# Kernel optimization log

Measured on AMD Instinct MI355X. Metric: run time of the kernel, lower is better.

## Reference

```python
import jax, jax.numpy as jnp
import numpy as np
import math

D_MODEL = 512
D_STATE = 16
D_CONV = 4
EXPAND = 2
N_LAYERS = 4
VOCAB = 30522
MAXLEN = 2048
NUM_LABELS = 2
D_INNER = EXPAND * D_MODEL  # 1024
DT_RANK = math.ceil(D_MODEL / 16)  # 32
B, S = 8, 2048


def setup_inputs() -> dict:
    key = jax.random.key(0)
    ks = jax.random.split(key, 12)
    n = lambda i, shape, s=0.02: jax.random.normal(ks[i], shape, jnp.float32) * s
    dt_std = DT_RANK ** -0.5
    return {
        "input_ids": jax.random.randint(ks[0], (B, S), 0, VOCAB),
        "attention_mask": jnp.ones((B, S), jnp.int32),
        "emb": n(1, (VOCAB, D_MODEL)),
        "pos_emb": n(2, (MAXLEN, D_MODEL)),
        "in_proj_w": n(3, (N_LAYERS, 2 * D_INNER, D_MODEL)),
        "conv_w": n(4, (N_LAYERS, D_INNER, D_CONV), 0.1),
        "conv_b": jnp.zeros((N_LAYERS, D_INNER), jnp.float32),
        "x_proj_w": n(5, (N_LAYERS, DT_RANK + 2 * D_STATE, D_INNER)),
        "dt_proj_w": jax.random.uniform(ks[6], (N_LAYERS, D_INNER, DT_RANK), jnp.float32, -dt_std, dt_std),
        "dt_proj_b": jnp.zeros((N_LAYERS, D_INNER), jnp.float32),
        "A_log": jnp.log(jnp.tile(jnp.arange(1, D_STATE + 1, dtype=jnp.float32), (N_LAYERS, D_INNER, 1))),
        "Dp": jnp.ones((N_LAYERS, D_INNER), jnp.float32),
        "out_proj_w": n(7, (N_LAYERS, D_MODEL, D_INNER)),
        "ln_g": jnp.ones((N_LAYERS, D_MODEL), jnp.float32),
        "ln_b": jnp.zeros((N_LAYERS, D_MODEL), jnp.float32),
        "fn_g": jnp.ones((D_MODEL,), jnp.float32),
        "fn_b": jnp.zeros((D_MODEL,), jnp.float32),
        "cls_w1": n(8, (D_MODEL, D_MODEL)),
        "cls_b1": jnp.zeros((D_MODEL,), jnp.float32),
        "cls_w2": n(9, (NUM_LABELS, D_MODEL)),
        "cls_b2": jnp.zeros((NUM_LABELS,), jnp.float32),
    }


def _layernorm(x, g, b, eps=1e-5):
    mu = jnp.mean(x, -1, keepdims=True)
    var = jnp.mean((x - mu) ** 2, -1, keepdims=True)
    return (x - mu) * jax.lax.rsqrt(var + eps) * g + b


def _mamba_block(x, in_w, cw, cb, xw, dtw, dtb, Alog, Dv, ow):
    # x: (B, S, d_model)
    xz = jnp.einsum('bsd,ed->bse', x, in_w)  # (B,S,2*d_inner)
    xi, z = jnp.split(xz, 2, axis=-1)
    # causal depthwise conv1d (left pad d_conv-1, valid conv)
    xp = jnp.pad(xi, ((0, 0), (D_CONV - 1, 0), (0, 0)))
    rhs = jnp.transpose(cw)[:, None, :]  # (d_conv, 1, d_inner)
    xc = jax.lax.conv_general_dilated(
        xp, rhs, (1,), 'VALID',
        dimension_numbers=('NWC', 'WIO', 'NWC'),
        feature_group_count=D_INNER) + cb
    xc = jax.nn.silu(xc)  # (B,S,d_inner)
    x_dbl = jnp.einsum('bsd,ed->bse', xc, xw)
    dt = x_dbl[..., :DT_RANK]
    Bm = x_dbl[..., DT_RANK:DT_RANK + D_STATE]
    Cm = x_dbl[..., DT_RANK + D_STATE:]
    dt = jax.nn.softplus(jnp.einsum('bsr,dr->bsd', dt, dtw) + dtb)  # (B,S,d_inner)
    A = -jnp.exp(Alog)  # (d_inner, d_state)

    def step(h, inp):
        x_t, dt_t, B_t, C_t = inp  # (B,d_inner),(B,d_inner),(B,d_state),(B,d_state)
        dA = jnp.exp(dt_t[:, :, None] * A[None])
        h = dA * h + (dt_t[:, :, None] * B_t[:, None, :]) * x_t[:, :, None]
        y_t = jnp.einsum('bds,bs->bd', h, C_t) + Dv * x_t
        return h, y_t

    h0 = jnp.zeros((x.shape[0], D_INNER, D_STATE), x.dtype)
    xs = (jnp.swapaxes(xc, 0, 1), jnp.swapaxes(dt, 0, 1),
          jnp.swapaxes(Bm, 0, 1), jnp.swapaxes(Cm, 0, 1))
    _, ys = jax.lax.scan(step, h0, xs)
    y = jnp.swapaxes(ys, 0, 1)  # (B,S,d_inner)
    y = y * jax.nn.silu(z)
    return jnp.einsum('bse,de->bsd', y, ow)


def reference(input_ids, attention_mask, emb, pos_emb, in_proj_w, conv_w, conv_b,
              x_proj_w, dt_proj_w, dt_proj_b, A_log, Dp, out_proj_w,
              ln_g, ln_b, fn_g, fn_b, cls_w1, cls_b1, cls_w2, cls_b2):
    seq_len = input_ids.shape[1]
    x = emb[input_ids] + pos_emb[:seq_len][None]
    for l in range(N_LAYERS):
        res = x
        x = _mamba_block(x, in_proj_w[l], conv_w[l], conv_b[l], x_proj_w[l],
                         dt_proj_w[l], dt_proj_b[l], A_log[l], Dp[l], out_proj_w[l])
        x = _layernorm(x + res, ln_g[l], ln_b[l])
    x = _layernorm(x, fn_g, fn_b)
    mask = attention_mask[:, :, None].astype(x.dtype)
    pooled = (x * mask).sum(1) / jnp.clip(mask.sum(1), 1e-9)
    h = jax.nn.gelu(pooled @ cls_w1.T + cls_b1, approximate=False)
    logits = h @ cls_w2.T + cls_b2
    return logits
```

## Files before the change

kernel.cpp:

```cpp
#include <hip/hip_runtime.h>
#include <math.h>

#define BATCH   8
#define S_LEN   2048
#define TOK     (BATCH*S_LEN)
#define DM      512
#define DI      1024
#define DST     16
#define DTR     32
#define NL      4
#define NLAB    2
#define NC      32
#define LC      (S_LEN/NC)

typedef _Float16 f16;
typedef _Float16 f16x8 __attribute__((ext_vector_type(8)));
typedef _Float16 f16x4 __attribute__((ext_vector_type(4)));
typedef float    f32x4 __attribute__((ext_vector_type(4)));

static constexpr size_t X_OFF     = 0;
static constexpr size_t XH_OFF    = 8388608;
static constexpr size_t XZH_OFF   = 12582912;
static constexpr size_t XCH_OFF   = 29360128;
static constexpr size_t XDBL_OFF  = 37748736;
static constexpr size_t DTH_OFF   = 38797312;
static constexpr size_t YH_OFF    = 47185920;
static constexpr size_t SDT_OFF   = 55574528;
static constexpr size_t WH_OFF    = 57802752;
static constexpr size_t XDH_OFF   = 61210624;
static constexpr size_t POOL_OFF  = 61734912;
static constexpr size_t H1_OFF    = POOL_OFF + 4096;

static constexpr size_t INWH_H  = 0;
static constexpr size_t XWH_H   = 4194304;
static constexpr size_t OWH_H   = 4456448;
static constexpr size_t DTWH_H  = 6553600;

__device__ __forceinline__ float softplus_fast(float x) {
    return fmaxf(x, 0.f) + __logf(1.f + __expf(-fabsf(x)));
}
__device__ __forceinline__ float silu_f(float x) {
    return x / (1.f + __expf(-x));
}

__device__ __forceinline__ void pow_tree(float w, float p[16]) {
    p[0] = w;           p[1] = w * w;       p[2] = p[1] * w;    p[3] = p[1] * p[1];
    p[4] = p[3] * w;    p[5] = p[3] * p[1]; p[6] = p[3] * p[2]; p[7] = p[3] * p[3];
    p[8] = p[7] * w;    p[9] = p[7] * p[1]; p[10] = p[7] * p[2]; p[11] = p[7] * p[3];
    p[12] = p[7] * p[4]; p[13] = p[7] * p[5]; p[14] = p[7] * p[6]; p[15] = p[7] * p[7];
}

__device__ __forceinline__ void gl_lds16(const void* g, void* l) {
    __builtin_amdgcn_global_load_lds(
        (const __attribute__((address_space(1))) void*)g,
        (__attribute__((address_space(3))) void*)l, 16, 0, 0);
}

__global__ __launch_bounds__(256)
void f2h_kernel(const float* __restrict__ src, f16* __restrict__ dst, int n8)
{
    int i = blockIdx.x * 256 + threadIdx.x;
    if (i >= n8) return;
    float4 a = ((const float4*)src)[i*2];
    float4 b = ((const float4*)src)[i*2+1];
    f16x8 o;
    o[0]=(f16)a.x; o[1]=(f16)a.y; o[2]=(f16)a.z; o[3]=(f16)a.w;
    o[4]=(f16)b.x; o[5]=(f16)b.y; o[6]=(f16)b.z; o[7]=(f16)b.w;
    *(f16x8*)(dst + (size_t)i*8) = o;
}

__global__ __launch_bounds__(256)
void dtw_pad_kernel(const float* __restrict__ src, f16* __restrict__ dst)
{
    int i = blockIdx.x * 256 + threadIdx.x;
    int c = i & 63;
    int row = i >> 6;
    dst[i] = (c < DTR) ? (f16)src[(size_t)row * DTR + c] : (f16)0.f;
}

__global__ __launch_bounds__(256)
void embed_kernel(const int* __restrict__ ids, const float* __restrict__ emb,
                  const float* __restrict__ pos, float* __restrict__ x,
                  f16* __restrict__ xh)
{
    int i = blockIdx.x * 256 + threadIdx.x;
    int t = i >> 7;
    int q = i & 127;
    int s = t & (S_LEN - 1);
    int id = ids[t];
    const float4 e = *(const float4*)(emb + ((size_t)id * DM) + q * 4);
    const float4 p = *(const float4*)(pos + ((size_t)s * DM) + q * 4);
    float4 o; o.x = e.x + p.x; o.y = e.y + p.y; o.z = e.z + p.z; o.w = e.w + p.w;
    *(float4*)(x + (size_t)t * DM + q * 4) = o;
    f16x4 h; h[0]=(f16)o.x; h[1]=(f16)o.y; h[2]=(f16)o.z; h[3]=(f16)o.w;
    *(f16x4*)(xh + (size_t)t * DM + q * 4) = h;
}

template<int BM,int BN,int EPI,typename OutT>
__global__ __launch_bounds__(256)
void gemm_h(const f16* __restrict__ A, const f16* __restrict__ B, OutT* __restrict__ C,
            const float* __restrict__ bias, f16* __restrict__ hcopy,
            int M, int N, int K, int lda, int ldb, int ldc)
{
    constexpr int BK = 64;
    constexpr int MI = BM / 32;
    constexpr int NI = BN / 32;
    __shared__ __align__(16) f16 As[2][BM * BK];
    __shared__ __align__(16) f16 Bs[2][BN * BK];

    const int tid  = threadIdx.x;
    const int wid  = tid >> 6, lane = tid & 63;
    const int wr   = wid >> 1, wc = wid & 1;
    const int m0   = blockIdx.x * BM, n0 = blockIdx.y * BN;
    const int srow = lane >> 3;
    const int scol = ((lane & 7) ^ (srow & 7)) * 8;
    constexpr int CPA = (BM / 8) / 4;
    constexpr int CPB = (BN / 8) / 4;

    f32x4 acc[MI][NI] = {};

    auto stage = [&](int buf, int kt) {
        #pragma unroll
        for (int i = 0; i < CPA; i++) {
            int ch = wid * CPA + i;
            gl_lds16(A + (size_t)(m0 + ch*8 + srow) * lda + kt + scol, &As[buf][ch*512]);
        }
        #pragma unroll
        for (int i = 0; i < CPB; i++) {
            int ch = wid * CPB + i;
            gl_lds16(B + (size_t)(n0 + ch*8 + srow) * ldb + kt + scol, &Bs[buf][ch*512]);
        }
    };
    auto compute = [&](int buf) {
        #pragma unroll
        for (int ks = 0; ks < 2; ks++) {
            f16x8 a[MI], b[NI];
            #pragma unroll
            for (int mi = 0; mi < MI; mi++) {
                int r = wr*MI*16 + mi*16 + (lane&15);
                int s = (ks*4 + (lane>>4)) ^ (r & 7);
                a[mi] = *(const f16x8*)(&As[buf][r*64 + s*8]);
            }
            #pragma unroll
            for (int ni = 0; ni < NI; ni++) {
                int r = wc*NI*16 + ni*16 + (lane&15);
                int s = (ks*4 + (lane>>4)) ^ (r & 7);
                b[ni] = *(const f16x8*)(&Bs[buf][r*64 + s*8]);
            }
            #pragma unroll
            for (int mi = 0; mi < MI; mi++)
                #pragma unroll
                for (int ni = 0; ni < NI; ni++)
                    acc[mi][ni] = __builtin_amdgcn_mfma_f32_16x16x32_f16(a[mi], b[ni], acc[mi][ni], 0, 0, 0);
        }
    };

    stage(0, 0);
    __syncthreads();
    int cur = 0;
    for (int kt = BK; kt < K; kt += BK) {
        stage(cur ^ 1, kt);
        compute(cur);
        __syncthreads();
        cur ^= 1;
    }
    compute(cur);

    const int cl = lane & 15, rh = lane >> 4;
    #pragma unroll
    for (int mi = 0; mi < MI; mi++) {
        #pragma unroll
        for (int ni = 0; ni < NI; ni++) {
            int col = n0 + wc*NI*16 + ni*16 + cl;
            #pragma unroll
            for (int r = 0; r < 4; r++) {
                int row = m0 + wr*MI*16 + mi*16 + rh*4 + r;
                float v = acc[mi][ni][r];
                if (EPI == 1) {
                    v = softplus_fast(v + bias[col]);
                    C[(size_t)row * ldc + col] = (OutT)v;
                } else {
                    C[(size_t)row * ldc + col] = (OutT)v;
                    if (EPI == 2) hcopy[(size_t)row * ldc + col] = (f16)v;
                }
            }
        }
    }
}

template<typename OutT>
__global__ __launch_bounds__(512)
void gemm_h8(const f16* __restrict__ A, const f16* __restrict__ B, OutT* __restrict__ C,
             int M, int N, int K, int lda, int ldb, int ldc, int nbn)
{
    constexpr int BK = 64;
    __shared__ __align__(16) f16 As[2][256 * BK];
    __shared__ __align__(16) f16 Bs[2][256 * BK];

    const int tid  = threadIdx.x;
    const int wid  = tid >> 6, lane = tid & 63;
    const int wr   = wid >> 2, wc = wid & 3;
    const int nwg = gridDim.x;
    const int xcd = blockIdx.x & 7, j = blockIdx.x >> 3;
    const int per_xcd_m = (nwg >> 3) / nbn;
    const int mblk = xcd * per_xcd_m + (j % per_xcd_m);
    const int nblk = j / per_xcd_m;
    const int m0 = mblk * 256, n0 = nblk * 256;

    const int srow = lane >> 3;
    const int scol = ((lane & 7) ^ (srow & 7)) * 8;

    f32x4 acc[8][4] = {};

    auto stage = [&](int buf, int kt) {
        #pragma unroll
        for (int i = 0; i < 4; i++) {
            int ch = wid * 4 + i;
            gl_lds16(A + (size_t)(m0 + ch*8 + srow) * lda + kt + scol, &As[buf][ch*512]);
        }
        #pragma unroll
        for (int i = 0; i < 4; i++) {
            int ch = wid * 4 + i;
            gl_lds16(B + (size_t)(n0 + ch*8 + srow) * ldb + kt + scol, &Bs[buf][ch*512]);
        }
    };
    auto compute = [&](int buf) {
        #pragma unroll
        for (int ks = 0; ks < 2; ks++) {
            f16x8 a[8], b[4];
            #pragma unroll
            for (int mi = 0; mi < 8; mi++) {
                int r = wr*128 + mi*16 + (lane&15);
                int s = (ks*4 + (lane>>4)) ^ (r & 7);
                a[mi] = *(const f16x8*)(&As[buf][r*64 + s*8]);
            }
            #pragma unroll
            for (int ni = 0; ni < 4; ni++) {
                int r = wc*64 + ni*16 + (lane&15);
                int s = (ks*4 + (lane>>4)) ^ (r & 7);
                b[ni] = *(const f16x8*)(&Bs[buf][r*64 + s*8]);
            }
            #pragma unroll
            for (int mi = 0; mi < 8; mi++)
                #pragma unroll
                for (int ni = 0; ni < 4; ni++)
                    acc[mi][ni] = __builtin_amdgcn_mfma_f32_16x16x32_f16(a[mi], b[ni], acc[mi][ni], 0, 0, 0);
        }
    };

    stage(0, 0);
    __syncthreads();
    int cur = 0;
    for (int kt = BK; kt < K; kt += BK) {
        stage(cur ^ 1, kt);
        compute(cur);
        __syncthreads();
        cur ^= 1;
    }
    compute(cur);

    const int cl = lane & 15, rh = lane >> 4;
    #pragma unroll
    for (int mi = 0; mi < 8; mi++) {
        #pragma unroll
        for (int ni = 0; ni < 4; ni++) {
            int col = n0 + wc*64 + ni*16 + cl;
            #pragma unroll
            for (int r = 0; r < 4; r++) {
                int row = m0 + wr*128 + mi*16 + rh*4 + r;
                C[(size_t)row * ldc + col] = (OutT)acc[mi][ni][r];
            }
        }
    }
}

__global__ __launch_bounds__(256)
void conv_h(const f16* __restrict__ xzh, const float* __restrict__ cw,
            const float* __restrict__ cb, f16* __restrict__ xch)
{
    int gid = blockIdx.x * 256 + threadIdx.x;
    int chunk = gid >> 7;
    int d0 = (gid & 127) * 8;
    int t0 = chunk * 8;
    bool first = (t0 & (S_LEN - 1)) == 0;

    float w[8][4];
    #pragma unroll
    for (int e = 0; e < 8; e++) {
        float4 wv = *(const float4*)(cw + (size_t)(d0 + e) * 4);
        w[e][0] = wv.x; w[e][1] = wv.y; w[e][2] = wv.z; w[e][3] = wv.w;
    }
    float bias[8];
    #pragma unroll
    for (int e = 0; e < 8; e += 4) {
        float4 bv = *(const float4*)(cb + d0 + e);
        bias[e] = bv.x; bias[e+1] = bv.y; bias[e+2] = bv.z; bias[e+3] = bv.w;
    }

    const f16* base = xzh + (size_t)t0 * 2048 + d0;
    f16x8 zero = {};
    f16x8 r0 = zero, r1 = zero, r2 = zero;
    if (!first) {
        r0 = *(const f16x8*)(base - 3 * 2048);
        r1 = *(const f16x8*)(base - 2 * 2048);
        r2 = *(const f16x8*)(base - 1 * 2048);
    }
    f16x8 cur = *(const f16x8*)base;
    f16* out = xch + (size_t)t0 * 1024 + d0;

    #pragma unroll
    for (int tt = 0; tt < 8; tt++) {
        f16x8 nxt = zero;
        if (tt < 7) nxt = *(const f16x8*)(base + (size_t)(tt + 1) * 2048);
        f16x8 o;
        #pragma unroll
        for (int e = 0; e < 8; e++) {
            float acc = bias[e];
            acc = fmaf(w[e][0], (float)r0[e], acc);
            acc = fmaf(w[e][1], (float)r1[e], acc);
            acc = fmaf(w[e][2], (float)r2[e], acc);
            acc = fmaf(w[e][3], (float)cur[e], acc);
            o[e] = (f16)silu_f(acc);
        }
        *(f16x8*)(out + (size_t)tt * 1024) = o;
        r0 = r1; r1 = r2; r2 = cur; cur = nxt;
    }
}

__global__ __launch_bounds__(256)
void scan_phase1(const f16* __restrict__ dth, const f16* __restrict__ xch,
                 const float* __restrict__ xdbl,
                 float* __restrict__ stateH, float* __restrict__ sdts)
{
    int blk  = blockIdx.x;
    int c    = blk % (NC - 1);
    int dgrp = (blk / (NC - 1)) & 3;
    int b    = blk / ((NC - 1) * 4);
    int tid  = threadIdx.x;
    int d    = dgrp * 256 + tid;

    __shared__ float Bs[LC][16];
    size_t tbase = (size_t)b * S_LEN + (size_t)c * LC;
    for (int i = tid; i < LC * 16; i += 256) {
        int t = i >> 4, n = i & 15;
        Bs[t][n] = xdbl[(tbase + t) * 64 + 32 + n];
    }
    __syncthreads();

    float h[16] = {};
    float sdt = 0.f;
    const f16* dtp = dth + tbase * 1024 + d;
    const f16* xvp = xch + tbase * 1024 + d;
    float dt_c = (float)dtp[0], xv_c = (float)xvp[0];
    for (int t = 0; t < LC; t++) {
        float dt_n = 0.f, xv_n = 0.f;
        if (t + 1 < LC) {
            dt_n = (float)dtp[(size_t)(t + 1) * 1024];
            xv_n = (float)xvp[(size_t)(t + 1) * 1024];
        }
        sdt += dt_c;
        float dtx = dt_c * xv_c;
        float p[16];
        pow_tree(__expf(-dt_c), p);
        #pragma unroll
        for (int n = 0; n < 16; n++)
            h[n] = fmaf(p[n], h[n], dtx * Bs[t][n]);
        dt_c = dt_n; xv_c = xv_n;
    }

    float* sp = stateH + (size_t)(b * NC + c) * 16 * 1024 + d;
    #pragma unroll
    for (int n = 0; n < 16; n++) sp[(size_t)n * 1024] = h[n];
    sdts[(size_t)(b * NC + c) * 1024 + d] = sdt;
}

__global__ __launch_bounds__(256)
void scan_phase2(float* __restrict__ stateH, const float* __restrict__ sdts)
{
    int gid = blockIdx.x * 256 + threadIdx.x;
    int d = gid & 1023;
    int n = (gid >> 10) & 15;
    int b = gid >> 14;
    float Ac = -(float)(n + 1);
    float h = 0.f;
    for (int c = 0; c < NC - 1; c++) {
        float* slot = stateH + ((size_t)(b * NC + c) * 16 + n) * 1024 + d;
        float hl = *slot;
        float sd = sdts[(size_t)(b * NC + c) * 1024 + d];
        *slot = h;
        h = fmaf(__expf(Ac * sd), h, hl);
    }
    stateH[((size_t)(b * NC + NC - 1) * 16 + n) * 1024 + d] = h;
}

__global__ __launch_bounds__(256)
void scan_phase3(const f16* __restrict__ dth, const f16* __restrict__ xch,
                 const f16* __restrict__ xzh, const float* __restrict__ xdbl,
                 const float* __restrict__ Dp, const float* __restrict__ stateH,
                 f16* __restrict__ yh)
{
    int blk  = blockIdx.x;
    int c    = blk % NC;
    int dgrp = (blk / NC) & 3;
    int b    = blk / (NC * 4);
    int tid  = threadIdx.x;
    int d    = dgrp * 256 + tid;

    __shared__ float Bs[LC][16];
    __shared__ float Cs[LC][16];
    size_t tbase = (size_t)b * S_LEN + (size_t)c * LC;
    for (int i = tid; i < LC * 16; i += 256) {
        int t = i >> 4, n = i & 15;
        Bs[t][n] = xdbl[(tbase + t) * 64 + 32 + n];
        Cs[t][n] = xdbl[(tbase + t) * 64 + 48 + n];
    }
    __syncthreads();

    const float* sp = stateH + (size_t)(b * NC + c) * 16 * 1024 + d;
    float h[16];
    #pragma unroll
    for (int n = 0; n < 16; n++) h[n] = sp[(size_t)n * 1024];
    float Dd = Dp[d];

    const f16* dtp = dth + tbase * 1024 + d;
    const f16* xvp = xch + tbase * 1024 + d;
    const f16* zp  = xzh + tbase * 2048 + 1024 + d;
    f16* yp = yh + tbase * 1024 + d;
    float dt_c = (float)dtp[0], xv_c = (float)xvp[0], z_c = (float)zp[0];
    for (int t = 0; t < LC; t++) {
        float dt_n = 0.f, xv_n = 0.f, z_n = 0.f;
        if (t + 1 < LC) {
            dt_n = (float)dtp[(size_t)(t + 1) * 1024];
            xv_n = (float)xvp[(size_t)(t + 1) * 1024];
            z_n  = (float)zp[(size_t)(t + 1) * 2048];
        }
        float dtx = dt_c * xv_c;
        float p[16];
        pow_tree(__expf(-dt_c), p);
        float y0 = Dd * xv_c, y1 = 0.f;
        #pragma unroll
        for (int n = 0; n < 16; n += 2) {
            h[n]   = fmaf(p[n],   h[n],   dtx * Bs[t][n]);
            h[n+1] = fmaf(p[n+1], h[n+1], dtx * Bs[t][n+1]);
            y0 = fmaf(h[n],   Cs[t][n],   y0);
            y1 = fmaf(h[n+1], Cs[t][n+1], y1);
        }
        yp[(size_t)t * 1024] = (f16)((y0 + y1) * silu_f(z_c));
        dt_c = dt_n; xv_c = xv_n; z_c = z_n;
    }
}

__global__ __launch_bounds__(256)
void ln_kernel(const float* __restrict__ inp, const float* __restrict__ res,
               float* __restrict__ outp, f16* __restrict__ hout,
               const float* __restrict__ g, const float* __restrict__ bta)
{
    size_t t = blockIdx.x;
    int tid = threadIdx.x;
    float v0 = inp[t * DM + tid];
    float v1 = inp[t * DM + tid + 256];
    if (res) { v0 += res[t * DM + tid]; v1 += res[t * DM + tid + 256]; }
    float s1 = v0 + v1, s2 = v0 * v0 + v1 * v1;
    #pragma unroll
    for (int m = 32; m; m >>= 1) { s1 += __shfl_xor(s1, m); s2 += __shfl_xor(s2, m); }
    __shared__ float r1[4], r2[4];
    if ((tid & 63) == 0) { r1[tid >> 6] = s1; r2[tid >> 6] = s2; }
    __syncthreads();
    float S1 = r1[0] + r1[1] + r1[2] + r1[3];
    float S2 = r2[0] + r2[1] + r2[2] + r2[3];
    float mu = S1 * (1.f / DM);
    float var = S2 * (1.f / DM) - mu * mu;
    float rstd = rsqrtf(var + 1e-5f);
    float o0 = (v0 - mu) * rstd * g[tid] + bta[tid];
    float o1 = (v1 - mu) * rstd * g[tid + 256] + bta[tid + 256];
    outp[t * DM + tid]       = o0;
    outp[t * DM + tid + 256] = o1;
    if (hout) {
        hout[t * DM + tid]       = (f16)o0;
        hout[t * DM + tid + 256] = (f16)o1;
    }
}

__global__ __launch_bounds__(512)
void pool_kernel(const float* __restrict__ x, const int* __restrict__ mask,
                 float* __restrict__ pooled)
{
    int b = blockIdx.x;
    int tid = threadIdx.x;
    __shared__ float mls[S_LEN];
    for (int s = tid; s < S_LEN; s += 512) mls[s] = (float)mask[(size_t)b * S_LEN + s];
    __syncthreads();
    float acc = 0.f, ms = 0.f;
    for (int s = 0; s < S_LEN; s++) {
        float m = mls[s];
        ms += m;
        acc = fmaf(x[((size_t)b * S_LEN + s) * DM + tid], m, acc);
    }
    pooled[(size_t)b * DM + tid] = acc / fmaxf(ms, 1e-9f);
}

__global__ __launch_bounds__(256)
void head1_kernel(const float* __restrict__ pooled, const float* __restrict__ w1,
                  const float* __restrict__ b1, float* __restrict__ h1)
{
    int out = blockIdx.x * 256 + threadIdx.x;
    int b = out >> 9, d = out & 511;
    float acc = b1[d];
    for (int k = 0; k < DM; k += 4) {
        float4 w = *(const float4*)(w1 + (size_t)d * DM + k);
        float4 p = *(const float4*)(pooled + (size_t)b * DM + k);
        acc = fmaf(w.x, p.x, acc); acc = fmaf(w.y, p.y, acc);
        acc = fmaf(w.z, p.z, acc); acc = fmaf(w.w, p.w, acc);
    }
    h1[out] = 0.5f * acc * (1.f + erff(acc * 0.70710678118654752f));
}

__global__ __launch_bounds__(256)
void head2_kernel(const float* __restrict__ h1, const float* __restrict__ w2,
                  const float* __restrict__ b2, float* __restrict__ logits)
{
    int tid = threadIdx.x;
    int grp = tid >> 4;
    int lane = tid & 15;
    int b = grp >> 1, c = grp & 1;
    float p = 0.f;
    for (int k = lane; k < DM; k += 16)
        p = fmaf(h1[(size_t)b * DM + k], w2[(size_t)c * DM + k], p);
    p += __shfl_xor(p, 1, 16);
    p += __shfl_xor(p, 2, 16);
    p += __shfl_xor(p, 4, 16);
    p += __shfl_xor(p, 8, 16);
    if (lane == 0) logits[grp] = p + b2[c];
}

extern "C" void kernel_launch(void* const* d_in, const int* in_sizes, int n_in,
                              void* d_out, int out_size, void* d_ws, size_t ws_size,
                              hipStream_t stream)
{
    const int*   ids    = (const int*)  d_in[0];
    const int*   amask  = (const int*)  d_in[1];
    const float* emb    = (const float*)d_in[2];
    const float* pos    = (const float*)d_in[3];
    const float* in_w   = (const float*)d_in[4];
    const float* conv_w = (const float*)d_in[5];
    const float* conv_b = (const float*)d_in[6];
    const float* x_w    = (const float*)d_in[7];
    const float* dt_w   = (const float*)d_in[8];
    const float* dt_b   = (const float*)d_in[9];
    const float* Dp     = (const float*)d_in[11];
    const float* out_w  = (const float*)d_in[12];
    const float* ln_g   = (const float*)d_in[13];
    const float* ln_b   = (const float*)d_in[14];
    const float* fn_g   = (const float*)d_in[15];
    const float* fn_b   = (const float*)d_in[16];
    const float* cls_w1 = (const float*)d_in[17];
    const float* cls_b1 = (const float*)d_in[18];
    const float* cls_w2 = (const float*)d_in[19];
    const float* cls_b2 = (const float*)d_in[20];

    float* ws     = (float*)d_ws;
    float* x      = ws + X_OFF;
    f16*   xh     = (f16*)(ws + XH_OFF);
    float* stateH = ws + XH_OFF;
    f16*   xzh    = (f16*)(ws + XZH_OFF);
    f16*   xch    = (f16*)(ws + XCH_OFF);
    float* xdbl   = ws + XDBL_OFF;
    f16*   dth    = (f16*)(ws + DTH_OFF);
    float* outtmp = ws + DTH_OFF;
    f16*   yh     = (f16*)(ws + YH_OFF);
    float* sdts   = ws + SDT_OFF;
    f16*   wh     = (f16*)(ws + WH_OFF);
    f16*   xdh    = (f16*)(ws + XDH_OFF);

    f2h_kernel<<<(NL*2048*512/8 + 255)/256, 256, 0, stream>>>(in_w,  wh + INWH_H, NL*2048*512/8);
    f2h_kernel<<<(NL*64*1024/8  + 255)/256, 256, 0, stream>>>(x_w,   wh + XWH_H,  NL*64*1024/8);
    f2h_kernel<<<(NL*512*1024/8 + 255)/256, 256, 0, stream>>>(out_w, wh + OWH_H,  NL*512*1024/8);
    dtw_pad_kernel<<<NL*1024*64/256, 256, 0, stream>>>(dt_w, wh + DTWH_H);

    embed_kernel<<<TOK * DM / 4 / 256, 256, 0, stream>>>(ids, emb, pos, x, xh);

    for (int l = 0; l < NL; l++) {
        const f16*   inwh = wh + INWH_H + (size_t)l * 2048 * 512;
        const f16*   xwh  = wh + XWH_H  + (size_t)l * 64 * 1024;
        const f16*   owh  = wh + OWH_H  + (size_t)l * 512 * 1024;
        const f16*   dtwh = wh + DTWH_H + (size_t)l * 1024 * 64;
        const float* cw   = conv_w + (size_t)l * DI * 4;
        const float* cb   = conv_b + (size_t)l * DI;
        const float* dtb  = dt_b   + (size_t)l * DI;
        const float* Dl   = Dp     + (size_t)l * DI;

        gemm_h8<f16><<<(TOK/256) * (2*DI/256), 512, 0, stream>>>(
            xh, inwh, xzh, TOK, 2*DI, DM, DM, DM, 2*DI, 2*DI/256);

        conv_h<<<(TOK/8) * 128 / 256, 256, 0, stream>>>(xzh, cw, cb, xch);

        gemm_h<64,64,2,float><<<dim3(TOK/64, 1), 256, 0, stream>>>(
            xch, xwh, xdbl, nullptr, xdh, TOK, 64, DI, DI, DI, 64);

        gemm_h<128,128,1,f16><<<dim3(TOK/128, DI/128), 256, 0, stream>>>(
            xdh, dtwh, dth, dtb, nullptr, TOK, DI, 64, 64, 64, DI);

        scan_phase1<<<BATCH * 4 * (NC - 1), 256, 0, stream>>>(dth, xch, xdbl, stateH, sdts);
        scan_phase2<<<BATCH * DI * DST / 256, 256, 0, stream>>>(stateH, sdts);
        scan_phase3<<<BATCH * 4 * NC, 256, 0, stream>>>(dth, xch, xzh, xdbl, Dl, stateH, yh);

        gemm_h<128,128,0,float><<<dim3(TOK/128, DM/128), 256, 0, stream>>>(
            yh, owh, outtmp, nullptr, nullptr, TOK, DM, DI, DI, DI, DM);

        ln_kernel<<<TOK, 256, 0, stream>>>(outtmp, x, x, xh,
                                           ln_g + (size_t)l*DM, ln_b + (size_t)l*DM);
    }

    ln_kernel<<<TOK, 256, 0, stream>>>(x, nullptr, x, nullptr, fn_g, fn_b);
    pool_kernel<<<BATCH, 512, 0, stream>>>(x, amask, ws + POOL_OFF);
    head1_kernel<<<BATCH * DM / 256, 256, 0, stream>>>(ws + POOL_OFF, cls_w1, cls_b1, ws + H1_OFF);
    head2_kernel<<<1, 256, 0, stream>>>(ws + H1_OFF, cls_w2, cls_b2, (float*)d_out);
}
```

Before: 1.055 ms.

## Prefetch GEMM tiles two stages ahead with explicit vmcnt waits; split pooling

The GEMM mainloops now issue the first two K-tiles up front. Each iteration waits on a partial vmcnt count instead of a full __syncthreads, so the next tile's global-to-LDS loads stay in flight during compute. Separately, the mean-pooling kernel, which ran only 8 blocks serially over 2048 tokens, is split into 128 partial-sum blocks plus a small reduce kernel to use more CUs. The hand-written vmcnt thresholds assume exact per-thread load counts, so a miscount could cause races.

```diff
diff --git a/kernel.cpp b/kernel.cpp
--- a/kernel.cpp
+++ b/kernel.cpp
@@ -56,6 +56,12 @@
         (__attribute__((address_space(3))) void*)l, 16, 0, 0);
 }
 
+#define WAIT_VM0() do { asm volatile("s_waitcnt vmcnt(0)" ::: "memory"); } while (0)
+#define WAIT_VM4() do { asm volatile("s_waitcnt vmcnt(4)" ::: "memory"); } while (0)
+#define WAIT_VM8() do { asm volatile("s_waitcnt vmcnt(8)" ::: "memory"); } while (0)
+#define SCHEDBAR() __builtin_amdgcn_sched_barrier(0)
+#define RAWBAR()   __builtin_amdgcn_s_barrier()
+
 __global__ __launch_bounds__(256)
 void f2h_kernel(const float* __restrict__ src, f16* __restrict__ dst, int n8)
 {
@@ -116,6 +122,7 @@
     const int scol = ((lane & 7) ^ (srow & 7)) * 8;
     constexpr int CPA = (BM / 8) / 4;
     constexpr int CPB = (BN / 8) / 4;
+    constexpr int LPS = CPA + CPB;
 
     f32x4 acc[MI][NI] = {};
 
@@ -155,16 +162,20 @@
         }
     };
 
+    const int nst = K / BK;
     stage(0, 0);
-    __syncthreads();
-    int cur = 0;
-    for (int kt = BK; kt < K; kt += BK) {
-        stage(cur ^ 1, kt);
+    if (nst > 1) stage(1, BK);
+    for (int s = 0; s < nst; s++) {
+        const int cur = s & 1;
+        if (s + 1 < nst) { if (LPS == 8) WAIT_VM8(); else WAIT_VM4(); }
+        else             { WAIT_VM0(); }
+        RAWBAR(); SCHEDBAR();
         compute(cur);
-        __syncthreads();
-        cur ^= 1;
-    }
-    compute(cur);
+        if (s + 2 < nst) {
+            RAWBAR(); SCHEDBAR();
+            stage(cur, (s + 2) * BK);
+        }
+    }
 
     const int cl = lane & 15, rh = lane >> 4;
     #pragma unroll
@@ -248,16 +259,19 @@
         }
     };
 
+    const int nst = K / BK;
     stage(0, 0);
-    __syncthreads();
-    int cur = 0;
-    for (int kt = BK; kt < K; kt += BK) {
-        stage(cur ^ 1, kt);
+    if (nst > 1) stage(1, BK);
+    for (int s = 0; s < nst; s++) {
+        const int cur = s & 1;
+        if (s + 1 < nst) WAIT_VM8(); else WAIT_VM0();
+        RAWBAR(); SCHEDBAR();
         compute(cur);
-        __syncthreads();
-        cur ^= 1;
-    }
-    compute(cur);
+        if (s + 2 < nst) {
+            RAWBAR(); SCHEDBAR();
+            stage(cur, (s + 2) * BK);
+        }
+    }
 
     const int cl = lane & 15, rh = lane >> 4;
     #pragma unroll
@@ -482,21 +496,45 @@
 }
 
 __global__ __launch_bounds__(512)
-void pool_kernel(const float* __restrict__ x, const int* __restrict__ mask,
+void pool_part(const float* __restrict__ x, const int* __restrict__ mask,
+               float* __restrict__ partial)
+{
+    int b = blockIdx.x >> 4;
+    int c = blockIdx.x & 15;
+    int tid = threadIdx.x;
+    __shared__ float mls[128];
+    if (tid < 128) mls[tid] = (float)mask[(size_t)b * S_LEN + c * 128 + tid];
+    __syncthreads();
+    const float* xp = x + ((size_t)b * S_LEN + (size_t)c * 128) * DM + tid;
+    float acc = 0.f;
+    #pragma unroll 4
+    for (int s = 0; s < 128; s++)
+        acc = fmaf(xp[(size_t)s * DM], mls[s], acc);
+    partial[(size_t)blockIdx.x * DM + tid] = acc;
+}
+
+__global__ __launch_bounds__(512)
+void pool_reduce(const float* __restrict__ partial, const int* __restrict__ mask,
                  float* __restrict__ pooled)
 {
     int b = blockIdx.x;
     int tid = threadIdx.x;
-    __shared__ float mls[S_LEN];
-    for (int s = tid; s < S_LEN; s += 512) mls[s] = (float)mask[(size_t)b * S_LEN + s];
+    float m4 = 0.f;
+    #pragma unroll
+    for (int q = 0; q < 4; q++)
+        m4 += (float)mask[(size_t)b * S_LEN + q * 512 + tid];
+    #pragma unroll
+    for (int off = 32; off; off >>= 1) m4 += __shfl_xor(m4, off);
+    __shared__ float r[8];
+    if ((tid & 63) == 0) r[tid >> 6] = m4;
     __syncthreads();
-    float acc = 0.f, ms = 0.f;
-    for (int s = 0; s < S_LEN; s++) {
-        float m = mls[s];
-        ms += m;
-        acc = fmaf(x[((size_t)b * S_LEN + s) * DM + tid], m, acc);
-    }
-    pooled[(size_t)b * DM + tid] = acc / fmaxf(ms, 1e-9f);
+    float msum = r[0]+r[1]+r[2]+r[3]+r[4]+r[5]+r[6]+r[7];
+
+    float acc = 0.f;
+    #pragma unroll
+    for (int c = 0; c < 16; c++)
+        acc += partial[((size_t)b * 16 + c) * DM + tid];
+    pooled[(size_t)b * DM + tid] = acc / fmaxf(msum, 1e-9f);
 }
 
 __global__ __launch_bounds__(256)
@@ -563,6 +601,7 @@
     f16*   xh     = (f16*)(ws + XH_OFF);
     float* stateH = ws + XH_OFF;
     f16*   xzh    = (f16*)(ws + XZH_OFF);
+    float* ppart  = ws + XZH_OFF;
     f16*   xch    = (f16*)(ws + XCH_OFF);
     float* xdbl   = ws + XDBL_OFF;
     f16*   dth    = (f16*)(ws + DTH_OFF);
@@ -612,7 +651,8 @@
     }
 
     ln_kernel<<<TOK, 256, 0, stream>>>(x, nullptr, x, nullptr, fn_g, fn_b);
-    pool_kernel<<<BATCH, 512, 0, stream>>>(x, amask, ws + POOL_OFF);
+    pool_part<<<BATCH * 16, 512, 0, stream>>>(x, amask, ppart);
+    pool_reduce<<<BATCH, 512, 0, stream>>>(ppart, amask, ws + POOL_OFF);
     head1_kernel<<<BATCH * DM / 256, 256, 0, stream>>>(ws + POOL_OFF, cls_w1, cls_b1, ws + H1_OFF);
     head2_kernel<<<1, 256, 0, stream>>>(ws + H1_OFF, cls_w2, cls_b2, (float*)d_out);
 }
```

New measurement: 1.000 ms. -5.2%, faster.
